# Optimization experiments

Hardware: AMD Instinct MI355X
Metric: run time of the kernel (lower is better)

Reference implementation:

```python
import jax, jax.numpy as jnp
import numpy as np

NUM_HEADS = 4
GROUPS = 8
EPS = 1e-5


def group_norm(x, w, b):
    B, C, H, W = x.shape
    xg = x.reshape(B, GROUPS, C // GROUPS, H, W)
    mu = jnp.mean(xg, axis=(2, 3, 4), keepdims=True)
    var = jnp.var(xg, axis=(2, 3, 4), keepdims=True)
    xg = (xg - mu) * jax.lax.rsqrt(var + EPS)
    x = xg.reshape(B, C, H, W)
    return x * w[None, :, None, None] + b[None, :, None, None]


def setup_inputs() -> dict:
    key = jax.random.key(0)
    k1, k2, k3 = jax.random.split(key, 3)
    B, C, H, W = 16, 256, 32, 32
    x = jax.random.normal(k1, (B, C, H, W), dtype=jnp.float32)
    gn_w = jnp.ones((C,), dtype=jnp.float32)
    gn_b = jnp.zeros((C,), dtype=jnp.float32)
    qkv_w = jax.random.normal(k2, (3 * C, C), dtype=jnp.float32) * 0.02
    qkv_b = jnp.zeros((3 * C,), dtype=jnp.float32)
    proj_w = jax.random.normal(k3, (C, C), dtype=jnp.float32) * 0.02
    proj_b = jnp.zeros((C,), dtype=jnp.float32)
    return {"x": x, "gn_w": gn_w, "gn_b": gn_b, "qkv_w": qkv_w,
            "qkv_b": qkv_b, "proj_w": proj_w, "proj_b": proj_b}


def reference(x, gn_w, gn_b, qkv_w, qkv_b, proj_w, proj_b):
    B, C, H, W = x.shape
    Dh = C // NUM_HEADS
    N = H * W
    skip = x
    xn = group_norm(x, gn_w, gn_b)
    # 1x1 conv QKV projection: [B,3C,H,W]
    qkv = jnp.einsum('oc,bchw->bohw', qkv_w, xn) + qkv_b[None, :, None, None]
    # split channel dim 3C -> [3, heads, Dh], flatten spatial -> N
    qkv = qkv.reshape(B, 3, NUM_HEADS, Dh, N)
    qkv = jnp.transpose(qkv, (1, 0, 2, 4, 3))  # [3,B,heads,N,Dh]
    q, k, v = qkv[0], qkv[1], qkv[2]
    scale = 1.0 / np.sqrt(Dh).astype(np.float32)
    attn = jnp.einsum('bhnd,bhmd->bhnm', q, k) * scale  # [B,heads,N,N]
    attn = jax.nn.softmax(attn, axis=-1)
    out = jnp.einsum('bhnm,bhmd->bhnd', attn, v)  # [B,heads,N,Dh]
    out = jnp.transpose(out, (0, 1, 3, 2)).reshape(B, C, H, W)
    out = jnp.einsum('oc,bchw->bohw', proj_w, out) + proj_b[None, :, None, None]
    return out + skip
```

## Files before the change

### kernel.cpp

```cpp
#include <hip/hip_runtime.h>

typedef unsigned short u16;
typedef __bf16 bf16x8 __attribute__((ext_vector_type(8)));
typedef float f32x4 __attribute__((ext_vector_type(4)));

#define QSCALE 0.18033688011112042f

__device__ __forceinline__ u16 f2bf(float f) {
  __bf16 h = (__bf16)f;
  union { __bf16 b; u16 u; } cv;
  cv.b = h;
  return cv.u;
}
__device__ __forceinline__ unsigned pack2(float a, float b) {
  return (unsigned)f2bf(a) | ((unsigned)f2bf(b) << 16);
}

__global__ __launch_bounds__(256) void convert_weights(
    const float* __restrict__ qw, const float* __restrict__ pw,
    u16* __restrict__ qwb, u16* __restrict__ pwb) {
  int i = blockIdx.x * 256 + threadIdx.x;
  const float* s; u16* d; int j;
  if (i < 49152) { s = qw; d = qwb; j = i; }
  else           { s = pw; d = pwb; j = i - 49152; }
  float4 v = *(const float4*)(s + (size_t)j * 4);
  uint2 o; o.x = pack2(v.x, v.y); o.y = pack2(v.z, v.w);
  *(uint2*)(d + (size_t)j * 4) = o;
}

__global__ __launch_bounds__(256) void gn_stats(const float* __restrict__ x,
                                                float* __restrict__ stats) {
  int bid = blockIdx.x;
  int t = threadIdx.x;
  int cl = t >> 3;
  int off = (t & 7) * 4;
  const float* p = x + (size_t)bid * 32768 + (size_t)cl * 1024 + off;
  float s = 0.f, ss = 0.f;
#pragma unroll 8
  for (int i = 0; i < 32; ++i) {
    float4 v = *(const float4*)(p + i * 32);
    s += v.x + v.y + v.z + v.w;
    ss += v.x * v.x + v.y * v.y + v.z * v.z + v.w * v.w;
  }
  __shared__ float sh1[256], sh2[256];
  sh1[t] = s; sh2[t] = ss;
  __syncthreads();
  for (int st = 128; st > 0; st >>= 1) {
    if (t < st) { sh1[t] += sh1[t + st]; sh2[t] += sh2[t + st]; }
    __syncthreads();
  }
  if (t == 0) {
    float mean = sh1[0] * (1.f / 32768.f);
    float var = sh2[0] * (1.f / 32768.f) - mean * mean;
    stats[bid * 2] = mean;
    stats[bid * 2 + 1] = rsqrtf(var + 1e-5f);
  }
}

__global__ __launch_bounds__(256) void gn_apply_t(
    const float* __restrict__ x, const float* __restrict__ stats,
    const float* __restrict__ gw, const float* __restrict__ gb,
    u16* __restrict__ xnt) {
  int bid = blockIdx.x;
  int b = bid >> 6, ct = (bid >> 4) & 3, nt = bid & 15;
  int c0 = ct * 64, n0 = nt * 64;
  int t = threadIdx.x;
  __shared__ float tile[64][65];
  {
    int cl = t >> 2, nc = (t & 3) * 16;
    int c = c0 + cl, g = c >> 5;
    float mu = stats[(b * 8 + g) * 2], rs = stats[(b * 8 + g) * 2 + 1];
    float w = gw[c] * rs, bb = gb[c] - mu * w;
    const float* p = x + ((size_t)(b * 256 + c)) * 1024 + n0 + nc;
#pragma unroll
    for (int i = 0; i < 16; i += 4) {
      float4 v = *(const float4*)(p + i);
      tile[cl][nc + i + 0] = v.x * w + bb;
      tile[cl][nc + i + 1] = v.y * w + bb;
      tile[cl][nc + i + 2] = v.z * w + bb;
      tile[cl][nc + i + 3] = v.w * w + bb;
    }
  }
  __syncthreads();
  int nl = t >> 2, cc = (t & 3) * 16;
  float v[16];
#pragma unroll
  for (int i = 0; i < 16; ++i) v[i] = tile[cc + i][nl];
  uint4 w0, w1;
  w0.x = pack2(v[0], v[1]);  w0.y = pack2(v[2], v[3]);
  w0.z = pack2(v[4], v[5]);  w0.w = pack2(v[6], v[7]);
  w1.x = pack2(v[8], v[9]);  w1.y = pack2(v[10], v[11]);
  w1.z = pack2(v[12], v[13]); w1.w = pack2(v[14], v[15]);
  u16* q = xnt + ((size_t)(b * 1024 + n0 + nl)) * 256 + c0 + cc;
  *(uint4*)q = w0;
  *(uint4*)(q + 8) = w1;
}

template <int EPI>
__global__ __launch_bounds__(256) void gemm_nt(
    const u16* __restrict__ A, const u16* __restrict__ Bm,
    const float* __restrict__ bias,
    u16* __restrict__ o_qt, u16* __restrict__ o_kt, u16* __restrict__ o_vn,
    const float* __restrict__ skip, float* __restrict__ out) {
  const int m0 = blockIdx.y * 128;
  const int n0 = blockIdx.x * 128;
  const int t = threadIdx.x;
  const int wave = t >> 6, lane = t & 63, lm = lane & 15, quad = lane >> 4;
  const int wr = wave >> 1, wc = wave & 1;

  __shared__ u16 As[128 * 32];
  __shared__ u16 Bs[128 * 32];

  f32x4 acc[4][4];
  const f32x4 fzero = {0.f, 0.f, 0.f, 0.f};
#pragma unroll
  for (int i = 0; i < 4; ++i)
#pragma unroll
    for (int j = 0; j < 4; ++j) acc[i][j] = fzero;

  const int srow = t >> 2, scol = (t & 3) * 8;

  for (int k0 = 0; k0 < 256; k0 += 32) {
    uint4 a0 = *(const uint4*)(A + (size_t)(m0 + srow) * 256 + k0 + scol);
    uint4 a1 = *(const uint4*)(A + (size_t)(m0 + 64 + srow) * 256 + k0 + scol);
    uint4 b0 = *(const uint4*)(Bm + (size_t)(n0 + srow) * 256 + k0 + scol);
    uint4 b1 = *(const uint4*)(Bm + (size_t)(n0 + 64 + srow) * 256 + k0 + scol);
    __syncthreads();
    *(uint4*)(As + srow * 32 + scol) = a0;
    *(uint4*)(As + (64 + srow) * 32 + scol) = a1;
    *(uint4*)(Bs + srow * 32 + scol) = b0;
    *(uint4*)(Bs + (64 + srow) * 32 + scol) = b1;
    __syncthreads();
    bf16x8 af[4], bf[4];
#pragma unroll
    for (int mb = 0; mb < 4; ++mb)
      af[mb] = *(const bf16x8*)(As + (wr * 64 + mb * 16 + lm) * 32 + quad * 8);
#pragma unroll
    for (int nb = 0; nb < 4; ++nb)
      bf[nb] = *(const bf16x8*)(Bs + (wc * 64 + nb * 16 + lm) * 32 + quad * 8);
#pragma unroll
    for (int mb = 0; mb < 4; ++mb)
#pragma unroll
      for (int nb = 0; nb < 4; ++nb)
        acc[mb][nb] = __builtin_amdgcn_mfma_f32_16x16x32_bf16(af[mb], bf[nb],
                                                              acc[mb][nb], 0, 0, 0);
  }

#pragma unroll
  for (int mb = 0; mb < 4; ++mb) {
#pragma unroll
    for (int nb = 0; nb < 4; ++nb) {
#pragma unroll
      for (int r = 0; r < 4; ++r) {
        const int o = m0 + wr * 64 + mb * 16 + 4 * quad + r;
        const int ng = n0 + wc * 64 + nb * 16 + lm;
        const float v = acc[mb][nb][r] + bias[o];
        const int b = ng >> 10, n = ng & 1023;
        if (EPI == 0) {
          const int oc = o & 255, h = oc >> 6, dd = oc & 63;
          const int kind = o >> 8;
          if (kind == 0)
            o_qt[((size_t)(b * 4 + h) * 1024 + n) * 64 + dd] = f2bf(v * QSCALE);
          else if (kind == 1)
            o_kt[((size_t)(b * 4 + h) * 1024 + n) * 64 + dd] = f2bf(v);
          else
            o_vn[((size_t)(b * 4 + h) * 64 + dd) * 1024 + n] = f2bf(v);
        } else {
          const size_t oi = ((size_t)(b * 256 + o)) * 1024 + n;
          out[oi] = v + skip[oi];
        }
      }
    }
  }
}

__global__ __launch_bounds__(256) void attn_fused(
    const u16* __restrict__ qt, const u16* __restrict__ kt,
    const u16* __restrict__ vn, u16* __restrict__ att) {
  const int bid = blockIdx.x;
  const int xcd = bid & 7, idx = bid >> 3;
  const int bh = xcd * 8 + (idx & 7);
  const int qtile = idx >> 3;
  const int t = threadIdx.x;
  const int wave = t >> 6, lane = t & 63, lm = lane & 15, quad = lane >> 4;

  const u16* qb = qt + (size_t)bh * (1024 * 64);
  const u16* kb = kt + (size_t)bh * (1024 * 64);
  const u16* vb = vn + (size_t)bh * (64 * 1024);

  const int i0 = qtile * 64 + wave * 16;
  const bf16x8 qf0 = *(const bf16x8*)(qb + (i0 + lm) * 64 + quad * 8);
  const bf16x8 qf1 = *(const bf16x8*)(qb + (i0 + lm) * 64 + 32 + quad * 8);

  __shared__ u16 Ks[64 * 64];
  __shared__ u16 Vs[64 * 64];
  __shared__ u16 Pl[4][16 * 72];

  const f32x4 fzero = {0.f, 0.f, 0.f, 0.f};
  f32x4 oacc[4];
#pragma unroll
  for (int d = 0; d < 4; ++d) oacc[d] = fzero;
  float lp[4] = {0.f, 0.f, 0.f, 0.f};

  const int e0 = t, e1 = t + 256;
  const int r0 = e0 >> 3, c0_ = e0 & 7, r1 = e1 >> 3, c1_ = e1 & 7;
  const int lk0 = r0 * 64 + ((c0_ ^ (r0 & 7)) * 8);
  const int lk1 = r1 * 64 + ((c1_ ^ (r1 & 7)) * 8);
  const u16* kg0 = kb + r0 * 64 + c0_ * 8;
  const u16* kg1 = kb + r1 * 64 + c1_ * 8;
  const u16* vg0 = vb + r0 * 1024 + c0_ * 8;
  const u16* vg1 = vb + r1 * 1024 + c1_ * 8;

  uint4 pk0 = *(const uint4*)kg0;
  uint4 pk1 = *(const uint4*)kg1;
  uint4 pv0 = *(const uint4*)vg0;
  uint4 pv1 = *(const uint4*)vg1;

  u16* pl = &Pl[wave][0];
  const int swz0 = (quad ^ (lm & 7)) * 8;
  const int swz1 = ((4 + quad) ^ (lm & 7)) * 8;

  for (int jc = 0; jc < 16; ++jc) {
    __syncthreads();
    *(uint4*)(Ks + lk0) = pk0;
    *(uint4*)(Ks + lk1) = pk1;
    *(uint4*)(Vs + lk0) = pv0;
    *(uint4*)(Vs + lk1) = pv1;
    __syncthreads();
    if (jc < 15) {
      pk0 = *(const uint4*)(kg0 + (jc + 1) * 4096);
      pk1 = *(const uint4*)(kg1 + (jc + 1) * 4096);
      pv0 = *(const uint4*)(vg0 + (jc + 1) * 64);
      pv1 = *(const uint4*)(vg1 + (jc + 1) * 64);
    }
    f32x4 sacc[4];
#pragma unroll
    for (int jb = 0; jb < 4; ++jb) sacc[jb] = fzero;
#pragma unroll
    for (int jb = 0; jb < 4; ++jb) {
      const int row = (jb * 16 + lm) * 64;
      bf16x8 kf0 = *(const bf16x8*)(Ks + row + swz0);
      bf16x8 kf1 = *(const bf16x8*)(Ks + row + swz1);
      sacc[jb] = __builtin_amdgcn_mfma_f32_16x16x32_bf16(qf0, kf0, sacc[jb], 0, 0, 0);
      sacc[jb] = __builtin_amdgcn_mfma_f32_16x16x32_bf16(qf1, kf1, sacc[jb], 0, 0, 0);
    }
#pragma unroll
    for (int jb = 0; jb < 4; ++jb) {
#pragma unroll
      for (int r = 0; r < 4; ++r) {
        const float p = exp2f(sacc[jb][r]);
        lp[r] += p;
        pl[(4 * quad + r) * 72 + jb * 16 + lm] = f2bf(p);
      }
    }
    bf16x8 pf0 = *(const bf16x8*)(pl + lm * 72 + quad * 8);
    bf16x8 pf1 = *(const bf16x8*)(pl + lm * 72 + 32 + quad * 8);
#pragma unroll
    for (int db = 0; db < 4; ++db) {
      const int row = (db * 16 + lm) * 64;
      bf16x8 vf0 = *(const bf16x8*)(Vs + row + swz0);
      bf16x8 vf1 = *(const bf16x8*)(Vs + row + swz1);
      oacc[db] = __builtin_amdgcn_mfma_f32_16x16x32_bf16(pf0, vf0, oacc[db], 0, 0, 0);
      oacc[db] = __builtin_amdgcn_mfma_f32_16x16x32_bf16(pf1, vf1, oacc[db], 0, 0, 0);
    }
  }

  const int b = bh >> 2, h = bh & 3;
#pragma unroll
  for (int r = 0; r < 4; ++r) {
    float rs = lp[r];
    rs += __shfl_xor(rs, 1);
    rs += __shfl_xor(rs, 2);
    rs += __shfl_xor(rs, 4);
    rs += __shfl_xor(rs, 8);
    const float inv = 1.f / rs;
    const int n = i0 + 4 * quad + r;
#pragma unroll
    for (int db = 0; db < 4; ++db) {
      const int c = h * 64 + db * 16 + lm;
      att[((size_t)(b * 1024 + n)) * 256 + c] = f2bf(oacc[db][r] * inv);
    }
  }
}

extern "C" void kernel_launch(void* const* d_in, const int* in_sizes, int n_in,
                              void* d_out, int out_size, void* d_ws, size_t ws_size,
                              hipStream_t stream) {
  const float* x      = (const float*)d_in[0];
  const float* gn_w   = (const float*)d_in[1];
  const float* gn_b   = (const float*)d_in[2];
  const float* qkv_w  = (const float*)d_in[3];
  const float* qkv_b  = (const float*)d_in[4];
  const float* proj_w = (const float*)d_in[5];
  const float* proj_b = (const float*)d_in[6];
  float* out = (float*)d_out;

  char* ws = (char*)d_ws;
  float* stats = (float*)(ws + 0);
  u16* qwb = (u16*)(ws + 4096);
  u16* pwb = (u16*)(ws + 397312);
  u16* xnt = (u16*)(ws + 528384);
  u16* qtb = (u16*)(ws + 8916992);
  u16* ktb = (u16*)(ws + 17305600);
  u16* vnb = (u16*)(ws + 25694208);
  u16* att = (u16*)(ws + 34082816);

  convert_weights<<<256, 256, 0, stream>>>(qkv_w, proj_w, qwb, pwb);
  gn_stats<<<128, 256, 0, stream>>>(x, stats);
  gn_apply_t<<<1024, 256, 0, stream>>>(x, stats, gn_w, gn_b, xnt);
  gemm_nt<0><<<dim3(128, 6), 256, 0, stream>>>(qwb, xnt, qkv_b, qtb, ktb, vnb,
                                               nullptr, nullptr);
  attn_fused<<<1024, 256, 0, stream>>>(qtb, ktb, vnb, att);
  gemm_nt<1><<<dim3(128, 2), 256, 0, stream>>>(pwb, att, proj_b, nullptr, nullptr,
                                               nullptr, x, out);
}
```

Measured before the change: 169.8 us.

## Merge prep kernels, double-buffer GEMM and attention, change QKV layouts

Merges weight conversion and group-norm statistics into one launch. Double-buffers the LDS tiles in the GEMM and in attention so each loop iteration needs one barrier instead of two, with global loads issued two steps ahead. Q and V are now stored d-major and K n-major with vectorized K stores. Attention computes S transposed (K as the A operand) so each lane writes P as one 4-wide store and keeps a single row-sum, and the Q tile is transposed into shared memory on load. The cost is more LDS per block, which may reduce occupancy, and scattered 2-byte scalar writes when staging Q.

```diff
diff --git a/kernel.cpp b/kernel.cpp
--- a/kernel.cpp
+++ b/kernel.cpp
@@ -16,22 +16,24 @@
   return (unsigned)f2bf(a) | ((unsigned)f2bf(b) << 16);
 }
 
-__global__ __launch_bounds__(256) void convert_weights(
+__global__ __launch_bounds__(256) void prep(
     const float* __restrict__ qw, const float* __restrict__ pw,
-    u16* __restrict__ qwb, u16* __restrict__ pwb) {
-  int i = blockIdx.x * 256 + threadIdx.x;
-  const float* s; u16* d; int j;
-  if (i < 49152) { s = qw; d = qwb; j = i; }
-  else           { s = pw; d = pwb; j = i - 49152; }
-  float4 v = *(const float4*)(s + (size_t)j * 4);
-  uint2 o; o.x = pack2(v.x, v.y); o.y = pack2(v.z, v.w);
-  *(uint2*)(d + (size_t)j * 4) = o;
-}
-
-__global__ __launch_bounds__(256) void gn_stats(const float* __restrict__ x,
-                                                float* __restrict__ stats) {
-  int bid = blockIdx.x;
-  int t = threadIdx.x;
+    const float* __restrict__ x,
+    u16* __restrict__ qwb, u16* __restrict__ pwb, float* __restrict__ stats) {
+  __shared__ float sh1[256], sh2[256];
+  const int blk = blockIdx.x;
+  const int t = threadIdx.x;
+  if (blk < 256) {
+    int i = blk * 256 + t;
+    const float* s; u16* d; int j;
+    if (i < 49152) { s = qw; d = qwb; j = i; }
+    else           { s = pw; d = pwb; j = i - 49152; }
+    float4 v = *(const float4*)(s + (size_t)j * 4);
+    uint2 o; o.x = pack2(v.x, v.y); o.y = pack2(v.z, v.w);
+    *(uint2*)(d + (size_t)j * 4) = o;
+    return;
+  }
+  const int bid = blk - 256;
   int cl = t >> 3;
   int off = (t & 7) * 4;
   const float* p = x + (size_t)bid * 32768 + (size_t)cl * 1024 + off;
@@ -42,7 +44,6 @@
     s += v.x + v.y + v.z + v.w;
     ss += v.x * v.x + v.y * v.y + v.z * v.z + v.w * v.w;
   }
-  __shared__ float sh1[256], sh2[256];
   sh1[t] = s; sh2[t] = ss;
   __syncthreads();
   for (int st = 128; st > 0; st >>= 1) {
@@ -100,7 +101,7 @@
 __global__ __launch_bounds__(256) void gemm_nt(
     const u16* __restrict__ A, const u16* __restrict__ Bm,
     const float* __restrict__ bias,
-    u16* __restrict__ o_qt, u16* __restrict__ o_kt, u16* __restrict__ o_vn,
+    u16* __restrict__ o_q, u16* __restrict__ o_k, u16* __restrict__ o_v,
     const float* __restrict__ skip, float* __restrict__ out) {
   const int m0 = blockIdx.y * 128;
   const int n0 = blockIdx.x * 128;
@@ -108,8 +109,8 @@
   const int wave = t >> 6, lane = t & 63, lm = lane & 15, quad = lane >> 4;
   const int wr = wave >> 1, wc = wave & 1;
 
-  __shared__ u16 As[128 * 32];
-  __shared__ u16 Bs[128 * 32];
+  __shared__ u16 As[2][128 * 32];
+  __shared__ u16 Bs[2][128 * 32];
 
   f32x4 acc[4][4];
   const f32x4 fzero = {0.f, 0.f, 0.f, 0.f};
@@ -119,25 +120,50 @@
     for (int j = 0; j < 4; ++j) acc[i][j] = fzero;
 
   const int srow = t >> 2, scol = (t & 3) * 8;
-
-  for (int k0 = 0; k0 < 256; k0 += 32) {
-    uint4 a0 = *(const uint4*)(A + (size_t)(m0 + srow) * 256 + k0 + scol);
-    uint4 a1 = *(const uint4*)(A + (size_t)(m0 + 64 + srow) * 256 + k0 + scol);
-    uint4 b0 = *(const uint4*)(Bm + (size_t)(n0 + srow) * 256 + k0 + scol);
-    uint4 b1 = *(const uint4*)(Bm + (size_t)(n0 + 64 + srow) * 256 + k0 + scol);
+  const u16* pA0 = A + (size_t)(m0 + srow) * 256 + scol;
+  const u16* pA1 = A + (size_t)(m0 + 64 + srow) * 256 + scol;
+  const u16* pB0 = Bm + (size_t)(n0 + srow) * 256 + scol;
+  const u16* pB1 = Bm + (size_t)(n0 + 64 + srow) * 256 + scol;
+
+  uint4 pa0 = *(const uint4*)pA0;
+  uint4 pa1 = *(const uint4*)pA1;
+  uint4 pb0 = *(const uint4*)pB0;
+  uint4 pb1 = *(const uint4*)pB1;
+  *(uint4*)(As[0] + srow * 32 + scol) = pa0;
+  *(uint4*)(As[0] + (64 + srow) * 32 + scol) = pa1;
+  *(uint4*)(Bs[0] + srow * 32 + scol) = pb0;
+  *(uint4*)(Bs[0] + (64 + srow) * 32 + scol) = pb1;
+  pa0 = *(const uint4*)(pA0 + 32);
+  pa1 = *(const uint4*)(pA1 + 32);
+  pb0 = *(const uint4*)(pB0 + 32);
+  pb1 = *(const uint4*)(pB1 + 32);
+
+  for (int ki = 0; ki < 8; ++ki) {
     __syncthreads();
-    *(uint4*)(As + srow * 32 + scol) = a0;
-    *(uint4*)(As + (64 + srow) * 32 + scol) = a1;
-    *(uint4*)(Bs + srow * 32 + scol) = b0;
-    *(uint4*)(Bs + (64 + srow) * 32 + scol) = b1;
-    __syncthreads();
+    if (ki + 1 < 8) {
+      u16* as = As[(ki + 1) & 1];
+      u16* bs = Bs[(ki + 1) & 1];
+      *(uint4*)(as + srow * 32 + scol) = pa0;
+      *(uint4*)(as + (64 + srow) * 32 + scol) = pa1;
+      *(uint4*)(bs + srow * 32 + scol) = pb0;
+      *(uint4*)(bs + (64 + srow) * 32 + scol) = pb1;
+    }
+    if (ki + 2 < 8) {
+      const int ko = (ki + 2) * 32;
+      pa0 = *(const uint4*)(pA0 + ko);
+      pa1 = *(const uint4*)(pA1 + ko);
+      pb0 = *(const uint4*)(pB0 + ko);
+      pb1 = *(const uint4*)(pB1 + ko);
+    }
+    const u16* as = As[ki & 1];
+    const u16* bs = Bs[ki & 1];
     bf16x8 af[4], bf[4];
 #pragma unroll
     for (int mb = 0; mb < 4; ++mb)
-      af[mb] = *(const bf16x8*)(As + (wr * 64 + mb * 16 + lm) * 32 + quad * 8);
+      af[mb] = *(const bf16x8*)(as + (wr * 64 + mb * 16 + lm) * 32 + quad * 8);
 #pragma unroll
     for (int nb = 0; nb < 4; ++nb)
-      bf[nb] = *(const bf16x8*)(Bs + (wc * 64 + nb * 16 + lm) * 32 + quad * 8);
+      bf[nb] = *(const bf16x8*)(bs + (wc * 64 + nb * 16 + lm) * 32 + quad * 8);
 #pragma unroll
     for (int mb = 0; mb < 4; ++mb)
 #pragma unroll
@@ -150,24 +176,33 @@
   for (int mb = 0; mb < 4; ++mb) {
 #pragma unroll
     for (int nb = 0; nb < 4; ++nb) {
-#pragma unroll
-      for (int r = 0; r < 4; ++r) {
-        const int o = m0 + wr * 64 + mb * 16 + 4 * quad + r;
-        const int ng = n0 + wc * 64 + nb * 16 + lm;
-        const float v = acc[mb][nb][r] + bias[o];
-        const int b = ng >> 10, n = ng & 1023;
-        if (EPI == 0) {
-          const int oc = o & 255, h = oc >> 6, dd = oc & 63;
-          const int kind = o >> 8;
-          if (kind == 0)
-            o_qt[((size_t)(b * 4 + h) * 1024 + n) * 64 + dd] = f2bf(v * QSCALE);
-          else if (kind == 1)
-            o_kt[((size_t)(b * 4 + h) * 1024 + n) * 64 + dd] = f2bf(v);
-          else
-            o_vn[((size_t)(b * 4 + h) * 64 + dd) * 1024 + n] = f2bf(v);
+      const int o = m0 + wr * 64 + mb * 16 + 4 * quad;
+      const int ng = n0 + wc * 64 + nb * 16 + lm;
+      const int b = ng >> 10, n = ng & 1023;
+      if (EPI == 0) {
+        const int kind = o >> 8;
+        if (kind == 1) {
+          ushort4 pk;
+          pk.x = f2bf(acc[mb][nb][0] + bias[o]);
+          pk.y = f2bf(acc[mb][nb][1] + bias[o + 1]);
+          pk.z = f2bf(acc[mb][nb][2] + bias[o + 2]);
+          pk.w = f2bf(acc[mb][nb][3] + bias[o + 3]);
+          const int h = (o >> 6) & 3;
+          *(ushort4*)(o_k + ((size_t)((b * 4 + h) * 1024 + n)) * 64 + (o & 63)) = pk;
         } else {
-          const size_t oi = ((size_t)(b * 256 + o)) * 1024 + n;
-          out[oi] = v + skip[oi];
+          u16* dst = (kind == 0) ? o_q : o_v;
+          const float sc = (kind == 0) ? QSCALE : 1.f;
+          const int oc = o & 255;
+#pragma unroll
+          for (int r = 0; r < 4; ++r)
+            dst[((size_t)(b * 256 + oc + r)) * 1024 + n] =
+                f2bf((acc[mb][nb][r] + bias[o + r]) * sc);
+        }
+      } else {
+#pragma unroll
+        for (int r = 0; r < 4; ++r) {
+          const size_t oi = ((size_t)(b * 256 + o + r)) * 1024 + n;
+          out[oi] = acc[mb][nb][r] + bias[o + r] + skip[oi];
         }
       }
     }
@@ -175,8 +210,8 @@
 }
 
 __global__ __launch_bounds__(256) void attn_fused(
-    const u16* __restrict__ qt, const u16* __restrict__ kt,
-    const u16* __restrict__ vn, u16* __restrict__ att) {
+    const u16* __restrict__ qdn, const u16* __restrict__ knd,
+    const u16* __restrict__ vdn, u16* __restrict__ att) {
   const int bid = blockIdx.x;
   const int xcd = bid & 7, idx = bid >> 3;
   const int bh = xcd * 8 + (idx & 7);
@@ -184,26 +219,15 @@
   const int t = threadIdx.x;
   const int wave = t >> 6, lane = t & 63, lm = lane & 15, quad = lane >> 4;
 
-  const u16* qb = qt + (size_t)bh * (1024 * 64);
-  const u16* kb = kt + (size_t)bh * (1024 * 64);
-  const u16* vb = vn + (size_t)bh * (64 * 1024);
-
-  const int i0 = qtile * 64 + wave * 16;
-  const bf16x8 qf0 = *(const bf16x8*)(qb + (i0 + lm) * 64 + quad * 8);
-  const bf16x8 qf1 = *(const bf16x8*)(qb + (i0 + lm) * 64 + 32 + quad * 8);
-
-  __shared__ u16 Ks[64 * 64];
-  __shared__ u16 Vs[64 * 64];
-  __shared__ u16 Pl[4][16 * 72];
-
-  const f32x4 fzero = {0.f, 0.f, 0.f, 0.f};
-  f32x4 oacc[4];
-#pragma unroll
-  for (int d = 0; d < 4; ++d) oacc[d] = fzero;
-  float lp[4] = {0.f, 0.f, 0.f, 0.f};
-
-  const int e0 = t, e1 = t + 256;
-  const int r0 = e0 >> 3, c0_ = e0 & 7, r1 = e1 >> 3, c1_ = e1 & 7;
+  const u16* qb = qdn + (size_t)bh * 65536;
+  const u16* kb = knd + (size_t)bh * 65536;
+  const u16* vb = vdn + (size_t)bh * 65536;
+
+  __shared__ u16 KV[2][2][64 * 64];
+  __shared__ u16 QP[64 * 64];
+
+  const int e1 = t + 256;
+  const int r0 = t >> 3, c0_ = t & 7, r1 = e1 >> 3, c1_ = e1 & 7;
   const int lk0 = r0 * 64 + ((c0_ ^ (r0 & 7)) * 8);
   const int lk1 = r1 * 64 + ((c1_ ^ (r1 & 7)) * 8);
   const u16* kg0 = kb + r0 * 64 + c0_ * 8;
@@ -216,23 +240,62 @@
   uint4 pv0 = *(const uint4*)vg0;
   uint4 pv1 = *(const uint4*)vg1;
 
-  u16* pl = &Pl[wave][0];
+  {
+    union { uint4 v; u16 s[8]; } tq0, tq1;
+    const int d0 = t >> 3, ngq = t & 7;
+    tq0.v = *(const uint4*)(qb + (size_t)d0 * 1024 + qtile * 64 + ngq * 8);
+    tq1.v = *(const uint4*)(qb + (size_t)(32 + d0) * 1024 + qtile * 64 + ngq * 8);
+    const int oa = d0 >> 3, ob = 4 + oa, dl = d0 & 7;
+#pragma unroll
+    for (int k = 0; k < 8; ++k) {
+      const int row = ngq * 8 + k;
+      QP[row * 64 + ((oa ^ k) * 8) + dl] = tq0.s[k];
+      QP[row * 64 + ((ob ^ k) * 8) + dl] = tq1.s[k];
+    }
+  }
+
+  *(uint4*)(KV[0][0] + lk0) = pk0;
+  *(uint4*)(KV[0][0] + lk1) = pk1;
+  *(uint4*)(KV[0][1] + lk0) = pv0;
+  *(uint4*)(KV[0][1] + lk1) = pv1;
+  pk0 = *(const uint4*)(kg0 + 4096);
+  pk1 = *(const uint4*)(kg1 + 4096);
+  pv0 = *(const uint4*)(vg0 + 64);
+  pv1 = *(const uint4*)(vg1 + 64);
+  __syncthreads();
+
+  const int qrow = wave * 16 + lm;
+  u16* Pw = QP + qrow * 64;
   const int swz0 = (quad ^ (lm & 7)) * 8;
   const int swz1 = ((4 + quad) ^ (lm & 7)) * 8;
+  const bf16x8 qf0 = *(const bf16x8*)(Pw + swz0);
+  const bf16x8 qf1 = *(const bf16x8*)(Pw + swz1);
+
+  const f32x4 fzero = {0.f, 0.f, 0.f, 0.f};
+  f32x4 oacc[4];
+#pragma unroll
+  for (int d = 0; d < 4; ++d) oacc[d] = fzero;
+  float lp = 0.f;
 
   for (int jc = 0; jc < 16; ++jc) {
-    __syncthreads();
-    *(uint4*)(Ks + lk0) = pk0;
-    *(uint4*)(Ks + lk1) = pk1;
-    *(uint4*)(Vs + lk0) = pv0;
-    *(uint4*)(Vs + lk1) = pv1;
-    __syncthreads();
-    if (jc < 15) {
-      pk0 = *(const uint4*)(kg0 + (jc + 1) * 4096);
-      pk1 = *(const uint4*)(kg1 + (jc + 1) * 4096);
-      pv0 = *(const uint4*)(vg0 + (jc + 1) * 64);
-      pv1 = *(const uint4*)(vg1 + (jc + 1) * 64);
-    }
+    if (jc) __syncthreads();
+    if (jc + 1 < 16) {
+      u16* kd = KV[(jc + 1) & 1][0];
+      u16* vd = KV[(jc + 1) & 1][1];
+      *(uint4*)(kd + lk0) = pk0;
+      *(uint4*)(kd + lk1) = pk1;
+      *(uint4*)(vd + lk0) = pv0;
+      *(uint4*)(vd + lk1) = pv1;
+    }
+    if (jc + 2 < 16) {
+      pk0 = *(const uint4*)(kg0 + (jc + 2) * 4096);
+      pk1 = *(const uint4*)(kg1 + (jc + 2) * 4096);
+      pv0 = *(const uint4*)(vg0 + (jc + 2) * 64);
+      pv1 = *(const uint4*)(vg1 + (jc + 2) * 64);
+    }
+    const u16* Ks = KV[jc & 1][0];
+    const u16* Vs = KV[jc & 1][1];
+
     f32x4 sacc[4];
 #pragma unroll
     for (int jb = 0; jb < 4; ++jb) sacc[jb] = fzero;
@@ -241,20 +304,23 @@
       const int row = (jb * 16 + lm) * 64;
       bf16x8 kf0 = *(const bf16x8*)(Ks + row + swz0);
       bf16x8 kf1 = *(const bf16x8*)(Ks + row + swz1);
-      sacc[jb] = __builtin_amdgcn_mfma_f32_16x16x32_bf16(qf0, kf0, sacc[jb], 0, 0, 0);
-      sacc[jb] = __builtin_amdgcn_mfma_f32_16x16x32_bf16(qf1, kf1, sacc[jb], 0, 0, 0);
+      sacc[jb] = __builtin_amdgcn_mfma_f32_16x16x32_bf16(kf0, qf0, sacc[jb], 0, 0, 0);
+      sacc[jb] = __builtin_amdgcn_mfma_f32_16x16x32_bf16(kf1, qf1, sacc[jb], 0, 0, 0);
     }
 #pragma unroll
     for (int jb = 0; jb < 4; ++jb) {
-#pragma unroll
-      for (int r = 0; r < 4; ++r) {
-        const float p = exp2f(sacc[jb][r]);
-        lp[r] += p;
-        pl[(4 * quad + r) * 72 + jb * 16 + lm] = f2bf(p);
-      }
-    }
-    bf16x8 pf0 = *(const bf16x8*)(pl + lm * 72 + quad * 8);
-    bf16x8 pf1 = *(const bf16x8*)(pl + lm * 72 + 32 + quad * 8);
+      const float e0 = exp2f(sacc[jb][0]);
+      const float e1_ = exp2f(sacc[jb][1]);
+      const float e2 = exp2f(sacc[jb][2]);
+      const float e3 = exp2f(sacc[jb][3]);
+      lp += (e0 + e1_) + (e2 + e3);
+      ushort4 pw4;
+      pw4.x = f2bf(e0); pw4.y = f2bf(e1_); pw4.z = f2bf(e2); pw4.w = f2bf(e3);
+      const int oct = 2 * jb + (quad >> 1);
+      *(ushort4*)(Pw + ((oct ^ (lm & 7)) * 8) + 4 * (quad & 1)) = pw4;
+    }
+    bf16x8 pf0 = *(const bf16x8*)(Pw + swz0);
+    bf16x8 pf1 = *(const bf16x8*)(Pw + swz1);
 #pragma unroll
     for (int db = 0; db < 4; ++db) {
       const int row = (db * 16 + lm) * 64;
@@ -265,16 +331,14 @@
     }
   }
 
+  float rs = lp;
+  rs += __shfl_xor(rs, 16);
+  rs += __shfl_xor(rs, 32);
   const int b = bh >> 2, h = bh & 3;
 #pragma unroll
   for (int r = 0; r < 4; ++r) {
-    float rs = lp[r];
-    rs += __shfl_xor(rs, 1);
-    rs += __shfl_xor(rs, 2);
-    rs += __shfl_xor(rs, 4);
-    rs += __shfl_xor(rs, 8);
-    const float inv = 1.f / rs;
-    const int n = i0 + 4 * quad + r;
+    const float inv = 1.f / __shfl(rs, 4 * quad + r);
+    const int n = qtile * 64 + wave * 16 + 4 * quad + r;
 #pragma unroll
     for (int db = 0; db < 4; ++db) {
       const int c = h * 64 + db * 16 + lm;
@@ -300,17 +364,16 @@
   u16* qwb = (u16*)(ws + 4096);
   u16* pwb = (u16*)(ws + 397312);
   u16* xnt = (u16*)(ws + 528384);
-  u16* qtb = (u16*)(ws + 8916992);
-  u16* ktb = (u16*)(ws + 17305600);
-  u16* vnb = (u16*)(ws + 25694208);
+  u16* qdn = (u16*)(ws + 8916992);
+  u16* knd = (u16*)(ws + 17305600);
+  u16* vdn = (u16*)(ws + 25694208);
   u16* att = (u16*)(ws + 34082816);
 
-  convert_weights<<<256, 256, 0, stream>>>(qkv_w, proj_w, qwb, pwb);
-  gn_stats<<<128, 256, 0, stream>>>(x, stats);
+  prep<<<384, 256, 0, stream>>>(qkv_w, proj_w, x, qwb, pwb, stats);
   gn_apply_t<<<1024, 256, 0, stream>>>(x, stats, gn_w, gn_b, xnt);
-  gemm_nt<0><<<dim3(128, 6), 256, 0, stream>>>(qwb, xnt, qkv_b, qtb, ktb, vnb,
+  gemm_nt<0><<<dim3(128, 6), 256, 0, stream>>>(qwb, xnt, qkv_b, qdn, knd, vdn,
                                                nullptr, nullptr);
-  attn_fused<<<1024, 256, 0, stream>>>(qtb, ktb, vnb, att);
+  attn_fused<<<1024, 256, 0, stream>>>(qdn, knd, vdn, att);
   gemm_nt<1><<<dim3(128, 2), 256, 0, stream>>>(pwb, att, proj_b, nullptr, nullptr,
                                                nullptr, x, out);
 }
```

Result: faster. 144.3 us (-15.1%).
